# Kernel optimization log

Hardware: AMD Instinct MI355X
Metric: run time of the kernel (lower is better)

Reference implementation:

```python
import jax, jax.numpy as jnp
import numpy as np

N = 50000
E = 800000
C = 128          # in = hidden = out channels
R = 16           # num_relations
NB = 4           # num_bases
EPS = 1e-5


def setup_inputs() -> dict:
    key = jax.random.key(0)
    ks = jax.random.split(key, 20)
    node_features = jax.random.normal(ks[0], (N, C), dtype=jnp.float32)
    src = jax.random.randint(ks[1], (E,), 0, N, dtype=jnp.int32)
    rel = jax.random.randint(ks[2], (E,), 0, R, dtype=jnp.int32)
    dst = jax.random.randint(ks[3], (E,), 0, N, dtype=jnp.int32)
    edge_triples = jnp.stack([src, rel, dst], axis=1)  # [E,3]
    s = 0.05
    inp = {
        "node_features": node_features,
        "edge_triples": edge_triples,
        "num_nodes": N,
        "input_w": jax.random.normal(ks[4], (C, C), jnp.float32) * s,
        "input_b": jnp.zeros((C,), jnp.float32),
    }
    for i in range(2):
        k = jax.random.split(ks[5 + i], 4)
        inp[f"basis{i}"] = jax.random.normal(k[0], (NB, C, C), jnp.float32) * s
        inp[f"att{i}"] = jax.random.normal(k[1], (R, NB), jnp.float32) * s
        inp[f"root_w{i}"] = jax.random.normal(k[2], (C, C), jnp.float32) * s
        inp[f"root_b{i}"] = jnp.zeros((C,), jnp.float32)
        inp[f"ln_g{i}"] = jnp.ones((C,), jnp.float32)
        inp[f"ln_b{i}"] = jnp.zeros((C,), jnp.float32)
    return inp


def _layer_norm(x, g, b):
    mu = jnp.mean(x, axis=-1, keepdims=True)
    var = jnp.mean(jnp.square(x - mu), axis=-1, keepdims=True)
    return (x - mu) * jax.lax.rsqrt(var + EPS) * g + b


def _rel_conv(x, edge_triples, num_nodes, basis, att, root_w, root_b):
    # x: [N,C]; basis: [NB,C,O]; att: [R,NB]
    src = edge_triples[:, 0]
    rel = edge_triples[:, 1]
    dst = edge_triples[:, 2]
    # weights = einsum('rb,bio->rio'); messages_e = x[src] @ weights[rel]
    # = sum_b att[rel,b] * (x @ basis[b])[src]  (same math, no [E,C,O] tensor)
    xb = jnp.einsum('ni,bio->bno', x, basis)      # [NB,N,O]
    coef = att[rel]                                # [E,NB]
    out_dim = basis.shape[-1]
    msg = jnp.zeros((src.shape[0], out_dim), x.dtype)
    for b in range(basis.shape[0]):                # small fixed loop over bases
        msg = msg + coef[:, b, None] * xb[b][src]
    deg = jax.ops.segment_sum(jnp.ones_like(dst, dtype=x.dtype), dst,
                              num_segments=num_nodes)
    deg_inv = jnp.where(deg > 0, 1.0 / deg, 0.0)
    msg = msg * deg_inv[dst][:, None]
    out = jax.ops.segment_sum(msg, dst, num_segments=num_nodes)
    return out + x @ root_w + root_b


def reference(node_features, edge_triples, num_nodes, input_w, input_b,
              basis0, att0, root_w0, root_b0, ln_g0, ln_b0,
              basis1, att1, root_w1, root_b1, ln_g1, ln_b1):
    x = node_features @ input_w + input_b
    x = _rel_conv(x, edge_triples, num_nodes, basis0, att0, root_w0, root_b0)
    x = _layer_norm(x, ln_g0, ln_b0)
    x = jax.nn.relu(x)  # dropout is identity in eval mode
    x = _rel_conv(x, edge_triples, num_nodes, basis1, att1, root_w1, root_b1)
    x = _layer_norm(x, ln_g1, ln_b1)
    return x
```

## Files before the change

### kernel.cpp

```cpp
#include <hip/hip_runtime.h>
#include <hip/hip_bf16.h>
#include <hip/hip_fp8.h>

#define NN 50000
#define EE 800000
#define NBLK 196

typedef __bf16 bf16x8 __attribute__((ext_vector_type(8)));
typedef float f32x4 __attribute__((ext_vector_type(4)));

__device__ inline float bf2f(unsigned int u) {
    union { unsigned int i; float f; } x; x.i = (u & 0xFFFFu) << 16; return x.f;
}
__device__ inline float bf2fh(unsigned int u) {
    union { unsigned int i; float f; } x; x.i = u & 0xFFFF0000u; return x.f;
}
__device__ inline void bf8_to_f(bf16x8 v, float* f) {
    const unsigned int* u = (const unsigned int*)&v;
    f[0] = bf2f(u[0]); f[1] = bf2fh(u[0]);
    f[2] = bf2f(u[1]); f[3] = bf2fh(u[1]);
    f[4] = bf2f(u[2]); f[5] = bf2fh(u[2]);
    f[6] = bf2f(u[3]); f[7] = bf2fh(u[3]);
}

__device__ inline void fp8x8_to_f(uint2 w, float* f) {
#if __has_builtin(__builtin_amdgcn_cvt_f32_fp8)
    f[0] = __builtin_amdgcn_cvt_f32_fp8(w.x, 0);
    f[1] = __builtin_amdgcn_cvt_f32_fp8(w.x, 1);
    f[2] = __builtin_amdgcn_cvt_f32_fp8(w.x, 2);
    f[3] = __builtin_amdgcn_cvt_f32_fp8(w.x, 3);
    f[4] = __builtin_amdgcn_cvt_f32_fp8(w.y, 0);
    f[5] = __builtin_amdgcn_cvt_f32_fp8(w.y, 1);
    f[6] = __builtin_amdgcn_cvt_f32_fp8(w.y, 2);
    f[7] = __builtin_amdgcn_cvt_f32_fp8(w.y, 3);
#else
    const unsigned char* b = (const unsigned char*)&w;
    #pragma unroll
    for (int j = 0; j < 8; ++j) { __hip_fp8_e4m3 v; v.__x = b[j]; f[j] = float(v); }
#endif
}
__device__ inline uint2 f8_pack(const float* f) {
#if __has_builtin(__builtin_amdgcn_cvt_pk_fp8_f32)
    unsigned int lo = __builtin_amdgcn_cvt_pk_fp8_f32(f[0], f[1], 0u, false);
    lo = __builtin_amdgcn_cvt_pk_fp8_f32(f[2], f[3], lo, true);
    unsigned int hi = __builtin_amdgcn_cvt_pk_fp8_f32(f[4], f[5], 0u, false);
    hi = __builtin_amdgcn_cvt_pk_fp8_f32(f[6], f[7], hi, true);
    return make_uint2(lo, hi);
#else
    unsigned char b[8];
    #pragma unroll
    for (int j = 0; j < 8; ++j) { __hip_fp8_e4m3 v(f[j]); b[j] = v.__x; }
    return *(uint2*)b;
#endif
}

__global__ void k_cvt8(const __bf16* __restrict__ in, unsigned char* __restrict__ out, int n8) {
    int i = blockIdx.x * 256 + threadIdx.x;
    if (i >= n8) return;
    bf16x8 v = ((const bf16x8*)in)[i];
    float f[8];
    bf8_to_f(v, f);
    ((uint2*)out)[i] = f8_pack(f);
}

__global__ void k_zero(int* __restrict__ deg, int* __restrict__ curs) {
    int i = blockIdx.x * 256 + threadIdx.x;
    if (i < NN) { deg[i] = 0; curs[i] = 0; }
}

__global__ void k_deg(const int* __restrict__ et, int* __restrict__ deg) {
    int e = blockIdx.x * 256 + threadIdx.x;
    if (e < EE) atomicAdd(&deg[et[e * 3 + 2]], 1);
}

__global__ void k_scan1(const int* __restrict__ deg, int* __restrict__ incl, int* __restrict__ bsum) {
    __shared__ int s[1024];
    int i = blockIdx.x * 1024 + threadIdx.x;
    int v = (i < NN) ? deg[i] : 0;
    s[threadIdx.x] = v;
    __syncthreads();
    for (int off = 1; off < 1024; off <<= 1) {
        int t = (threadIdx.x >= off) ? s[threadIdx.x - off] : 0;
        __syncthreads();
        s[threadIdx.x] += t;
        __syncthreads();
    }
    if (i < NN) incl[i] = s[threadIdx.x];
    if (threadIdx.x == 1023) bsum[blockIdx.x] = s[1023];
}

__global__ void k_scan2(const int* __restrict__ bsum, int* __restrict__ boff) {
    if (threadIdx.x == 0 && blockIdx.x == 0) {
        int acc = 0;
        for (int i = 0; i < 49; ++i) { boff[i] = acc; acc += bsum[i]; }
    }
}

__global__ void k_scan3(const int* __restrict__ incl, const int* __restrict__ deg,
                        const int* __restrict__ boff, int* __restrict__ row_start) {
    int i = blockIdx.x * 1024 + threadIdx.x;
    if (i < NN) row_start[i] = incl[i] - deg[i] + boff[blockIdx.x];
}

__global__ void k_fill(const int* __restrict__ et, const int* __restrict__ row_start,
                       int* __restrict__ cursor, int* __restrict__ perm) {
    int e = blockIdx.x * 256 + threadIdx.x;
    if (e >= EE) return;
    int src = et[e * 3 + 0];
    int rel = et[e * 3 + 1];
    int dst = et[e * 3 + 2];
    int pos = row_start[dst] + atomicAdd(&cursor[dst], 1);
    perm[pos] = src | (rel << 16);
}

__global__ void k_prep(const float* __restrict__ iw,
                       const float* __restrict__ basis0, const float* __restrict__ rootw0,
                       const float* __restrict__ basis1, const float* __restrict__ rootw1,
                       __bf16* __restrict__ WtInF, __bf16* __restrict__ WtF0, __bf16* __restrict__ WtF1) {
    int t = blockIdx.x * 256 + threadIdx.x;
    if (t < 2048) {
        int lane = t & 63, grp = t >> 6;
        int kk = grp & 3, nblk = grp >> 2;
        int col = nblk * 16 + (lane & 15);
        int k0 = kk * 32 + (lane >> 4) * 8;
        bf16x8 v;
        #pragma unroll
        for (int j = 0; j < 8; ++j) v[j] = (__bf16)iw[(size_t)(k0 + j) * 128 + col];
        *(bf16x8*)(WtInF + (size_t)t * 8) = v;
        return;
    }
    t -= 2048;
    const float* basis = basis0; const float* rootw = rootw0; __bf16* W = WtF0;
    if (t >= 10240) { t -= 10240; basis = basis1; rootw = rootw1; W = WtF1; }
    if (t >= 10240) return;
    int lane = t & 63, grp = t >> 6;
    int kk = grp % 20, nblk = grp / 20;
    int col = nblk * 16 + (lane & 15);
    int k0 = kk * 32 + (lane >> 4) * 8;
    bf16x8 v;
    #pragma unroll
    for (int j = 0; j < 8; ++j) {
        int k = k0 + j;
        float f = (k < 512) ? basis[(size_t)(k >> 7) * 16384 + (size_t)(k & 127) * 128 + col]
                            : rootw[(size_t)(k - 512) * 128 + col];
        v[j] = (__bf16)f;
    }
    *(bf16x8*)(W + (size_t)t * 8) = v;
}

__global__ void k_gemm_in(const float* __restrict__ A, const __bf16* __restrict__ WtInF,
                          const float* __restrict__ bias, __bf16* __restrict__ out, int M) {
    const int tid = threadIdx.x, wave = tid >> 6, lane = tid & 63;
    const int wr = wave >> 1, wc = wave & 1;
    const int l15 = lane & 15, lhi = lane >> 4;
    f32x4 acc[2][4] = {};
    #define LDAI(dst, KK) do { \
        _Pragma("unroll") \
        for (int m = 0; m < 2; ++m) { \
            int rw = blockIdx.x * 64 + wr * 32 + m * 16 + l15; \
            rw = rw < M ? rw : M - 1; \
            const float* ap = A + (size_t)rw * 128 + (KK) * 32 + lhi * 8; \
            float4 v0 = *(const float4*)ap, v1 = *(const float4*)(ap + 4); \
            bf16x8 f; \
            f[0]=(__bf16)v0.x; f[1]=(__bf16)v0.y; f[2]=(__bf16)v0.z; f[3]=(__bf16)v0.w; \
            f[4]=(__bf16)v1.x; f[5]=(__bf16)v1.y; f[6]=(__bf16)v1.z; f[7]=(__bf16)v1.w; \
            dst[m] = f; \
        } } while (0)
    #define LDBI(dst, KK) do { \
        _Pragma("unroll") \
        for (int n = 0; n < 4; ++n) \
            dst[n] = *(const bf16x8*)(WtInF + (((size_t)(wc * 4 + n) * 4 + (KK)) * 64 + lane) * 8); \
        } while (0)
    #define MMI(AA, BB) do { \
        _Pragma("unroll") for (int m = 0; m < 2; ++m) \
        _Pragma("unroll") for (int n = 0; n < 4; ++n) \
            acc[m][n] = __builtin_amdgcn_mfma_f32_16x16x32_bf16(AA[m], BB[n], acc[m][n], 0, 0, 0); \
        } while (0)
    bf16x8 aP[2], bP[4], aQ[2], bQ[4];
    LDAI(aP, 0); LDBI(bP, 0);
    #pragma unroll
    for (int tstep = 0; tstep < 2; ++tstep) {
        LDAI(aQ, 2 * tstep + 1); LDBI(bQ, 2 * tstep + 1);
        MMI(aP, bP);
        if (tstep < 1) { LDAI(aP, 2 * tstep + 2); LDBI(bP, 2 * tstep + 2); }
        MMI(aQ, bQ);
    }
    #pragma unroll
    for (int m = 0; m < 2; ++m)
        #pragma unroll
        for (int j = 0; j < 4; ++j) {
            int row = blockIdx.x * 64 + wr * 32 + m * 16 + lhi * 4 + j;
            if (row >= M) continue;
            #pragma unroll
            for (int n = 0; n < 4; ++n) {
                int col = wc * 64 + n * 16 + l15;
                out[(size_t)row * 128 + col] = (__bf16)(acc[m][n][j] + bias[col]);
            }
        }
}

__global__ void k_agg7(const unsigned char* __restrict__ x8, const int* __restrict__ perm,
                       const int* __restrict__ rowst, const int* __restrict__ deg,
                       const float* __restrict__ att, __bf16* __restrict__ aggF,
                       int nodeOff, int nodeCnt) {
    __shared__ float4 satt[16];
    if (threadIdx.x < 16) satt[threadIdx.x] = ((const float4*)att)[threadIdx.x];
    __syncthreads();
    int local = blockIdx.x * 4 + (threadIdx.x >> 6);
    if (local >= nodeCnt) return;
    int lane = threadIdx.x & 63;
    int e4 = lane >> 4, c8 = lane & 15;
    int node = nodeOff + local;
    int start = rowst[node], cnt = deg[node];
    float acc[4][8] = {};
    int nIt = (cnt + 3) >> 2;
    for (int it = 0; it < nIt; it += 2) {
        int eA = it * 4 + e4, eB = eA + 4;
        bool vA = eA < cnt, vB = eB < cnt;
        int pA = vA ? perm[start + eA] : 0;
        int pB = vB ? perm[start + eB] : 0;
        uint2 uA = *(const uint2*)(x8 + (size_t)(pA & 0xFFFF) * 128 + c8 * 8);
        uint2 uB = *(const uint2*)(x8 + (size_t)(pB & 0xFFFF) * 128 + c8 * 8);
        float4 cA = vA ? satt[pA >> 16] : make_float4(0.f, 0.f, 0.f, 0.f);
        float4 cB = vB ? satt[pB >> 16] : make_float4(0.f, 0.f, 0.f, 0.f);
        float fA[8], fB[8];
        fp8x8_to_f(uA, fA);
        fp8x8_to_f(uB, fB);
        #pragma unroll
        for (int j = 0; j < 8; ++j) {
            acc[0][j] += cA.x * fA[j]; acc[1][j] += cA.y * fA[j];
            acc[2][j] += cA.z * fA[j]; acc[3][j] += cA.w * fA[j];
        }
        #pragma unroll
        for (int j = 0; j < 8; ++j) {
            acc[0][j] += cB.x * fB[j]; acc[1][j] += cB.y * fB[j];
            acc[2][j] += cB.z * fB[j]; acc[3][j] += cB.w * fB[j];
        }
    }
    float dinv = (cnt > 0) ? 1.f / (float)cnt : 0.f;
    #pragma unroll
    for (int b = 0; b < 4; ++b)
        #pragma unroll
        for (int j = 0; j < 8; ++j) {
            float v = acc[b][j];
            v += __shfl_xor(v, 16);
            v += __shfl_xor(v, 32);
            acc[b][j] = v * dinv;
        }
    bf16x8 o;
    #pragma unroll
    for (int j = 0; j < 8; ++j) {
        float v = (e4 == 0) ? acc[0][j] : (e4 == 1) ? acc[1][j] : (e4 == 2) ? acc[2][j] : acc[3][j];
        o[j] = (__bf16)v;
    }
    size_t idx8 = (((size_t)(local >> 4) * 16 + e4 * 4 + (c8 >> 2)) * 64 + (c8 & 3) * 16 + (local & 15)) * 8;
    *(bf16x8*)(aggF + idx8) = o;
}

template<int OUTF>
__global__ void k_gemm_layer(const __bf16* __restrict__ aggF, const __bf16* __restrict__ x,
                             const __bf16* __restrict__ WtF, const float* __restrict__ rb,
                             const float* __restrict__ g, const float* __restrict__ bb,
                             __bf16* __restrict__ outB, float* __restrict__ outF,
                             int rowOff, int nodeCnt) {
    __shared__ float red[2][2][64];
    __shared__ float murs[2][64];
    const int tid = threadIdx.x, wave = tid >> 6, lane = tid & 63;
    const int wr = wave >> 1, wc = wave & 1;
    const int l15 = lane & 15, lhi = lane >> 4;
    const int rowgrpBase = blockIdx.x * 4 + wr * 2;
    f32x4 acc[2][4] = {};
    #define LDA(dst, KK) do { \
        _Pragma("unroll") \
        for (int m = 0; m < 2; ++m) { \
            if ((KK) < 16) { \
                dst[m] = *(const bf16x8*)(aggF + (((size_t)(rowgrpBase + m) * 16 + (KK)) * 64 + lane) * 8); \
            } else { \
                int rw = blockIdx.x * 64 + wr * 32 + m * 16 + l15; \
                rw = rw < nodeCnt ? rw : nodeCnt - 1; \
                dst[m] = *(const bf16x8*)(x + (size_t)(rowOff + rw) * 128 + ((KK) - 16) * 32 + lhi * 8); \
            } \
        } } while (0)
    #define LDB(dst, KK) do { \
        _Pragma("unroll") \
        for (int n = 0; n < 4; ++n) \
            dst[n] = *(const bf16x8*)(WtF + (((size_t)(wc * 4 + n) * 20 + (KK)) * 64 + lane) * 8); \
        } while (0)
    #define MM(AA, BB) do { \
        _Pragma("unroll") for (int m = 0; m < 2; ++m) \
        _Pragma("unroll") for (int n = 0; n < 4; ++n) \
            acc[m][n] = __builtin_amdgcn_mfma_f32_16x16x32_bf16(AA[m], BB[n], acc[m][n], 0, 0, 0); \
        } while (0)
    bf16x8 aP[2], bP[4], aQ[2], bQ[4];
    LDA(aP, 0); LDB(bP, 0);
    #pragma unroll
    for (int t = 0; t < 10; ++t) {
        LDA(aQ, 2 * t + 1); LDB(bQ, 2 * t + 1);
        MM(aP, bP);
        if (t < 9) { LDA(aP, 2 * t + 2); LDB(bP, 2 * t + 2); }
        MM(aQ, bQ);
    }
    float colb[4];
    #pragma unroll
    for (int n = 0; n < 4; ++n) colb[n] = rb[wc * 64 + n * 16 + l15];
    #pragma unroll
    for (int m = 0; m < 2; ++m)
        #pragma unroll
        for (int j = 0; j < 4; ++j) {
            float s = 0.f, q = 0.f;
            #pragma unroll
            for (int n = 0; n < 4; ++n) {
                float v = acc[m][n][j] + colb[n];
                acc[m][n][j] = v;
                s += v; q += v * v;
            }
            #pragma unroll
            for (int o = 1; o < 16; o <<= 1) { s += __shfl_xor(s, o); q += __shfl_xor(q, o); }
            if (l15 == 0) {
                int r = wr * 32 + m * 16 + lhi * 4 + j;
                red[0][wc][r] = s; red[1][wc][r] = q;
            }
        }
    __syncthreads();
    if (tid < 64) {
        float s = red[0][0][tid] + red[0][1][tid];
        float q = red[1][0][tid] + red[1][1][tid];
        float mu = s * (1.f / 128.f);
        float var = q * (1.f / 128.f) - mu * mu;
        murs[0][tid] = mu;
        murs[1][tid] = rsqrtf(var + 1e-5f);
    }
    __syncthreads();
    float gg[4], gb[4];
    #pragma unroll
    for (int n = 0; n < 4; ++n) {
        int col = wc * 64 + n * 16 + l15;
        gg[n] = g[col]; gb[n] = bb[col];
    }
    #pragma unroll
    for (int m = 0; m < 2; ++m)
        #pragma unroll
        for (int j = 0; j < 4; ++j) {
            int rblk = wr * 32 + m * 16 + lhi * 4 + j;
            int lr = blockIdx.x * 64 + rblk;
            if (lr >= nodeCnt) continue;
            float mu = murs[0][rblk], rs = murs[1][rblk];
            size_t rowbase = (size_t)(rowOff + lr) * 128;
            #pragma unroll
            for (int n = 0; n < 4; ++n) {
                int col = wc * 64 + n * 16 + l15;
                float v = (acc[m][n][j] - mu) * rs * gg[n] + gb[n];
                if (OUTF == 0) { v = fmaxf(v, 0.f); outB[rowbase + col] = (__bf16)v; }
                else           { outF[rowbase + col] = v; }
            }
        }
}

extern "C" void kernel_launch(void* const* d_in, const int* in_sizes, int n_in,
                              void* d_out, int out_size, void* d_ws, size_t ws_size,
                              hipStream_t stream) {
    const float* nf      = (const float*)d_in[0];
    const int*   et      = (const int*)d_in[1];
    const float* input_w = (const float*)d_in[3];
    const float* input_b = (const float*)d_in[4];
    const float* basis0  = (const float*)d_in[5];
    const float* att0    = (const float*)d_in[6];
    const float* rootw0  = (const float*)d_in[7];
    const float* rootb0  = (const float*)d_in[8];
    const float* lng0    = (const float*)d_in[9];
    const float* lnb0    = (const float*)d_in[10];
    const float* basis1  = (const float*)d_in[11];
    const float* att1    = (const float*)d_in[12];
    const float* rootw1  = (const float*)d_in[13];
    const float* rootb1  = (const float*)d_in[14];
    const float* lng1    = (const float*)d_in[15];
    const float* lnb1    = (const float*)d_in[16];
    (void)in_sizes; (void)n_in; (void)out_size;

    char* ws = (char*)d_ws;
    size_t off = 0;
    auto carve = [&](size_t bytes) { char* p = ws + off; off = (off + bytes + 255) & ~(size_t)255; return p; };
    __bf16* x0    = (__bf16*)carve((size_t)NN * 128 * 2);
    __bf16* x1    = (__bf16*)carve((size_t)NN * 128 * 2);
    unsigned char* x08 = (unsigned char*)carve((size_t)NN * 128);
    unsigned char* x18 = (unsigned char*)carve((size_t)NN * 128);
    __bf16* WtInF = (__bf16*)carve((size_t)128 * 128 * 2);
    __bf16* WtF0  = (__bf16*)carve((size_t)128 * 640 * 2);
    __bf16* WtF1  = (__bf16*)carve((size_t)128 * 640 * 2);
    int*    deg   = (int*)carve((size_t)NN * 4);
    int*    incl  = (int*)carve((size_t)NN * 4);
    int*    rowst = (int*)carve((size_t)NN * 4);
    int*    curs  = (int*)carve((size_t)NN * 4);
    int*    bsum  = (int*)carve(64 * 4);
    int*    boff  = (int*)carve(64 * 4);
    int*    perm  = (int*)carve((size_t)EE * 4 + 64);
    size_t remain = (ws_size > off + 4096) ? (ws_size - off - 4096) : 0;
    long long maxNodes = (long long)(remain / 1024);
    int chunkN = (maxNodes >= NN) ? NN : (int)maxNodes;
    if (chunkN < 512) chunkN = 512;
    chunkN = (chunkN + 63) & ~63;
    __bf16* aggF = (__bf16*)carve((size_t)chunkN * 512 * 2);
    int nch = (NN + chunkN - 1) / chunkN;

    k_zero<<<NBLK, 256, 0, stream>>>(deg, curs);
    k_deg<<<(EE + 255) / 256, 256, 0, stream>>>(et, deg);
    k_scan1<<<49, 1024, 0, stream>>>(deg, incl, bsum);
    k_scan2<<<1, 64, 0, stream>>>(bsum, boff);
    k_scan3<<<49, 1024, 0, stream>>>(incl, deg, boff, rowst);
    k_fill<<<(EE + 255) / 256, 256, 0, stream>>>(et, rowst, curs, perm);

    k_prep<<<88, 256, 0, stream>>>(input_w, basis0, rootw0, basis1, rootw1, WtInF, WtF0, WtF1);
    k_gemm_in<<<(NN + 63) / 64, 256, 0, stream>>>(nf, WtInF, input_b, x0, NN);
    k_cvt8<<<(NN * 16 + 255) / 256, 256, 0, stream>>>(x0, x08, NN * 16);

    for (int c = 0; c < nch; ++c) {
        int o0 = c * chunkN;
        int cnt = (o0 + chunkN <= NN) ? chunkN : (NN - o0);
        k_agg7<<<(cnt + 3) / 4, 256, 0, stream>>>(x08, perm, rowst, deg, att0, aggF, o0, cnt);
        k_gemm_layer<0><<<(cnt + 63) / 64, 256, 0, stream>>>(aggF, x0, WtF0, rootb0, lng0, lnb0,
                                                             x1, nullptr, o0, cnt);
    }
    k_cvt8<<<(NN * 16 + 255) / 256, 256, 0, stream>>>(x1, x18, NN * 16);

    for (int c = 0; c < nch; ++c) {
        int o0 = c * chunkN;
        int cnt = (o0 + chunkN <= NN) ? chunkN : (NN - o0);
        k_agg7<<<(cnt + 3) / 4, 256, 0, stream>>>(x18, perm, rowst, deg, att1, aggF, o0, cnt);
        k_gemm_layer<1><<<(cnt + 63) / 64, 256, 0, stream>>>(aggF, x1, WtF1, rootb1, lng1, lnb1,
                                                             nullptr, (float*)d_out, o0, cnt);
    }
}
```

Baseline: 268.4 us.

## Fuse edge aggregation and basis GEMM with LayerNorm into one kernel

Merges the per-node fp8 gather/aggregation kernel and the MFMA GEMM+LayerNorm kernel into a single kernel per layer. Each 256-thread block aggregates 32 nodes into a shared-memory tile in MFMA fragment layout, then runs the GEMM and LayerNorm directly from LDS. This removes the global round-trip of the aggregated buffer and the chunked launch loop. In exchange, the GEMM tile per block shrinks from 64 to 32 rows, so weight fragments are reloaded twice as often, and about 33 KB of LDS per block limits occupancy.

```diff
diff --git a/kernel.cpp b/kernel.cpp
--- a/kernel.cpp
+++ b/kernel.cpp
@@ -199,130 +199,133 @@
         }
 }
 
-__global__ void k_agg7(const unsigned char* __restrict__ x8, const int* __restrict__ perm,
-                       const int* __restrict__ rowst, const int* __restrict__ deg,
-                       const float* __restrict__ att, __bf16* __restrict__ aggF,
-                       int nodeOff, int nodeCnt) {
+template<int OUTF>
+__global__ void __launch_bounds__(256, 4)
+k_fused(const unsigned char* __restrict__ x8, const __bf16* __restrict__ x,
+        const __bf16* __restrict__ WtF,
+        const int* __restrict__ perm, const int* __restrict__ rowst,
+        const int* __restrict__ deg, const float* __restrict__ att,
+        const float* __restrict__ rb, const float* __restrict__ g,
+        const float* __restrict__ bb,
+        __bf16* __restrict__ outB, float* __restrict__ outF)
+{
+    __shared__ __attribute__((aligned(16))) __bf16 aggL[32 * 512];
     __shared__ float4 satt[16];
-    if (threadIdx.x < 16) satt[threadIdx.x] = ((const float4*)att)[threadIdx.x];
+    __shared__ float red[2][2][32];
+    __shared__ float murs[2][32];
+    const int tid = threadIdx.x, wave = tid >> 6, lane = tid & 63;
+    if (tid < 16) satt[tid] = ((const float4*)att)[tid];
     __syncthreads();
-    int local = blockIdx.x * 4 + (threadIdx.x >> 6);
-    if (local >= nodeCnt) return;
-    int lane = threadIdx.x & 63;
-    int e4 = lane >> 4, c8 = lane & 15;
-    int node = nodeOff + local;
-    int start = rowst[node], cnt = deg[node];
-    float acc[4][8] = {};
-    int nIt = (cnt + 3) >> 2;
-    for (int it = 0; it < nIt; it += 2) {
-        int eA = it * 4 + e4, eB = eA + 4;
-        bool vA = eA < cnt, vB = eB < cnt;
-        int pA = vA ? perm[start + eA] : 0;
-        int pB = vB ? perm[start + eB] : 0;
-        uint2 uA = *(const uint2*)(x8 + (size_t)(pA & 0xFFFF) * 128 + c8 * 8);
-        uint2 uB = *(const uint2*)(x8 + (size_t)(pB & 0xFFFF) * 128 + c8 * 8);
-        float4 cA = vA ? satt[pA >> 16] : make_float4(0.f, 0.f, 0.f, 0.f);
-        float4 cB = vB ? satt[pB >> 16] : make_float4(0.f, 0.f, 0.f, 0.f);
-        float fA[8], fB[8];
-        fp8x8_to_f(uA, fA);
-        fp8x8_to_f(uB, fB);
-        #pragma unroll
-        for (int j = 0; j < 8; ++j) {
-            acc[0][j] += cA.x * fA[j]; acc[1][j] += cA.y * fA[j];
-            acc[2][j] += cA.z * fA[j]; acc[3][j] += cA.w * fA[j];
-        }
-        #pragma unroll
-        for (int j = 0; j < 8; ++j) {
-            acc[0][j] += cB.x * fB[j]; acc[1][j] += cB.y * fB[j];
-            acc[2][j] += cB.z * fB[j]; acc[3][j] += cB.w * fB[j];
-        }
-    }
-    float dinv = (cnt > 0) ? 1.f / (float)cnt : 0.f;
-    #pragma unroll
-    for (int b = 0; b < 4; ++b)
-        #pragma unroll
-        for (int j = 0; j < 8; ++j) {
-            float v = acc[b][j];
-            v += __shfl_xor(v, 16);
-            v += __shfl_xor(v, 32);
-            acc[b][j] = v * dinv;
-        }
-    bf16x8 o;
-    #pragma unroll
-    for (int j = 0; j < 8; ++j) {
-        float v = (e4 == 0) ? acc[0][j] : (e4 == 1) ? acc[1][j] : (e4 == 2) ? acc[2][j] : acc[3][j];
-        o[j] = (__bf16)v;
-    }
-    size_t idx8 = (((size_t)(local >> 4) * 16 + e4 * 4 + (c8 >> 2)) * 64 + (c8 & 3) * 16 + (local & 15)) * 8;
-    *(bf16x8*)(aggF + idx8) = o;
-}
-
-template<int OUTF>
-__global__ void k_gemm_layer(const __bf16* __restrict__ aggF, const __bf16* __restrict__ x,
-                             const __bf16* __restrict__ WtF, const float* __restrict__ rb,
-                             const float* __restrict__ g, const float* __restrict__ bb,
-                             __bf16* __restrict__ outB, float* __restrict__ outF,
-                             int rowOff, int nodeCnt) {
-    __shared__ float red[2][2][64];
-    __shared__ float murs[2][64];
-    const int tid = threadIdx.x, wave = tid >> 6, lane = tid & 63;
+    const int e4 = lane >> 4, c8 = lane & 15;
+    const int blockBase = blockIdx.x * 32;
+
+    for (int i = 0; i < 8; ++i) {
+        int local = wave * 8 + i;
+        int node = blockBase + local;
+        bf16x8 o;
+        #pragma unroll
+        for (int j = 0; j < 8; ++j) o[j] = (__bf16)0.f;
+        if (node < NN) {
+            int start = rowst[node], cnt = deg[node];
+            float acc[4][8] = {};
+            int nIt = (cnt + 3) >> 2;
+            for (int it = 0; it < nIt; it += 2) {
+                int eA = it * 4 + e4, eB = eA + 4;
+                bool vA = eA < cnt, vB = eB < cnt;
+                int pA = vA ? perm[start + eA] : 0;
+                int pB = vB ? perm[start + eB] : 0;
+                uint2 uA = *(const uint2*)(x8 + (size_t)(pA & 0xFFFF) * 128 + c8 * 8);
+                uint2 uB = *(const uint2*)(x8 + (size_t)(pB & 0xFFFF) * 128 + c8 * 8);
+                float4 cA = vA ? satt[pA >> 16] : make_float4(0.f, 0.f, 0.f, 0.f);
+                float4 cB = vB ? satt[pB >> 16] : make_float4(0.f, 0.f, 0.f, 0.f);
+                float fA[8], fB[8];
+                fp8x8_to_f(uA, fA);
+                fp8x8_to_f(uB, fB);
+                #pragma unroll
+                for (int j = 0; j < 8; ++j) {
+                    acc[0][j] += cA.x * fA[j]; acc[1][j] += cA.y * fA[j];
+                    acc[2][j] += cA.z * fA[j]; acc[3][j] += cA.w * fA[j];
+                }
+                #pragma unroll
+                for (int j = 0; j < 8; ++j) {
+                    acc[0][j] += cB.x * fB[j]; acc[1][j] += cB.y * fB[j];
+                    acc[2][j] += cB.z * fB[j]; acc[3][j] += cB.w * fB[j];
+                }
+            }
+            float dinv = (cnt > 0) ? 1.f / (float)cnt : 0.f;
+            #pragma unroll
+            for (int b = 0; b < 4; ++b)
+                #pragma unroll
+                for (int j = 0; j < 8; ++j) {
+                    float v = acc[b][j];
+                    v += __shfl_xor(v, 16);
+                    v += __shfl_xor(v, 32);
+                    acc[b][j] = v * dinv;
+                }
+            #pragma unroll
+            for (int j = 0; j < 8; ++j) {
+                float v = (e4 == 0) ? acc[0][j] : (e4 == 1) ? acc[1][j]
+                        : (e4 == 2) ? acc[2][j] : acc[3][j];
+                o[j] = (__bf16)v;
+            }
+        }
+        int idx8 = (((local >> 4) * 16 + e4 * 4 + (c8 >> 2)) * 64 + (c8 & 3) * 16 + (local & 15)) * 8;
+        *(bf16x8*)(aggL + idx8) = o;
+    }
+    __syncthreads();
+
     const int wr = wave >> 1, wc = wave & 1;
     const int l15 = lane & 15, lhi = lane >> 4;
-    const int rowgrpBase = blockIdx.x * 4 + wr * 2;
-    f32x4 acc[2][4] = {};
-    #define LDA(dst, KK) do { \
-        _Pragma("unroll") \
-        for (int m = 0; m < 2; ++m) { \
-            if ((KK) < 16) { \
-                dst[m] = *(const bf16x8*)(aggF + (((size_t)(rowgrpBase + m) * 16 + (KK)) * 64 + lane) * 8); \
-            } else { \
-                int rw = blockIdx.x * 64 + wr * 32 + m * 16 + l15; \
-                rw = rw < nodeCnt ? rw : nodeCnt - 1; \
-                dst[m] = *(const bf16x8*)(x + (size_t)(rowOff + rw) * 128 + ((KK) - 16) * 32 + lhi * 8); \
-            } \
+    f32x4 acc2[4] = {};
+    #define FLDA(dst, KK) do { \
+        if ((KK) < 16) { \
+            dst = *(const bf16x8*)(aggL + ((wr * 16 + (KK)) * 64 + lane) * 8); \
+        } else { \
+            int nd = blockBase + wr * 16 + l15; \
+            nd = nd < NN ? nd : NN - 1; \
+            dst = *(const bf16x8*)(x + (size_t)nd * 128 + ((KK) - 16) * 32 + lhi * 8); \
         } } while (0)
-    #define LDB(dst, KK) do { \
+    #define FLDB(dst, KK) do { \
         _Pragma("unroll") \
         for (int n = 0; n < 4; ++n) \
             dst[n] = *(const bf16x8*)(WtF + (((size_t)(wc * 4 + n) * 20 + (KK)) * 64 + lane) * 8); \
         } while (0)
-    #define MM(AA, BB) do { \
-        _Pragma("unroll") for (int m = 0; m < 2; ++m) \
+    #define FMM(AA, BB) do { \
         _Pragma("unroll") for (int n = 0; n < 4; ++n) \
-            acc[m][n] = __builtin_amdgcn_mfma_f32_16x16x32_bf16(AA[m], BB[n], acc[m][n], 0, 0, 0); \
+            acc2[n] = __builtin_amdgcn_mfma_f32_16x16x32_bf16(AA, BB[n], acc2[n], 0, 0, 0); \
         } while (0)
-    bf16x8 aP[2], bP[4], aQ[2], bQ[4];
-    LDA(aP, 0); LDB(bP, 0);
-    #pragma unroll
-    for (int t = 0; t < 10; ++t) {
-        LDA(aQ, 2 * t + 1); LDB(bQ, 2 * t + 1);
-        MM(aP, bP);
-        if (t < 9) { LDA(aP, 2 * t + 2); LDB(bP, 2 * t + 2); }
-        MM(aQ, bQ);
+    {
+        bf16x8 aP, bP[4], aQ, bQ[4];
+        FLDA(aP, 0); FLDB(bP, 0);
+        #pragma unroll
+        for (int t = 0; t < 10; ++t) {
+            FLDA(aQ, 2 * t + 1); FLDB(bQ, 2 * t + 1);
+            FMM(aP, bP);
+            if (t < 9) { FLDA(aP, 2 * t + 2); FLDB(bP, 2 * t + 2); }
+            FMM(aQ, bQ);
+        }
     }
     float colb[4];
     #pragma unroll
     for (int n = 0; n < 4; ++n) colb[n] = rb[wc * 64 + n * 16 + l15];
     #pragma unroll
-    for (int m = 0; m < 2; ++m)
-        #pragma unroll
-        for (int j = 0; j < 4; ++j) {
-            float s = 0.f, q = 0.f;
-            #pragma unroll
-            for (int n = 0; n < 4; ++n) {
-                float v = acc[m][n][j] + colb[n];
-                acc[m][n][j] = v;
-                s += v; q += v * v;
-            }
-            #pragma unroll
-            for (int o = 1; o < 16; o <<= 1) { s += __shfl_xor(s, o); q += __shfl_xor(q, o); }
-            if (l15 == 0) {
-                int r = wr * 32 + m * 16 + lhi * 4 + j;
-                red[0][wc][r] = s; red[1][wc][r] = q;
-            }
-        }
+    for (int j = 0; j < 4; ++j) {
+        float s = 0.f, q = 0.f;
+        #pragma unroll
+        for (int n = 0; n < 4; ++n) {
+            float v = acc2[n][j] + colb[n];
+            acc2[n][j] = v;
+            s += v; q += v * v;
+        }
+        #pragma unroll
+        for (int o = 1; o < 16; o <<= 1) { s += __shfl_xor(s, o); q += __shfl_xor(q, o); }
+        if (l15 == 0) {
+            int r = wr * 16 + lhi * 4 + j;
+            red[0][wc][r] = s; red[1][wc][r] = q;
+        }
+    }
     __syncthreads();
-    if (tid < 64) {
+    if (tid < 32) {
         float s = red[0][0][tid] + red[0][1][tid];
         float q = red[1][0][tid] + red[1][1][tid];
         float mu = s * (1.f / 128.f);
@@ -338,22 +341,20 @@
         gg[n] = g[col]; gb[n] = bb[col];
     }
     #pragma unroll
-    for (int m = 0; m < 2; ++m)
-        #pragma unroll
-        for (int j = 0; j < 4; ++j) {
-            int rblk = wr * 32 + m * 16 + lhi * 4 + j;
-            int lr = blockIdx.x * 64 + rblk;
-            if (lr >= nodeCnt) continue;
-            float mu = murs[0][rblk], rs = murs[1][rblk];
-            size_t rowbase = (size_t)(rowOff + lr) * 128;
-            #pragma unroll
-            for (int n = 0; n < 4; ++n) {
-                int col = wc * 64 + n * 16 + l15;
-                float v = (acc[m][n][j] - mu) * rs * gg[n] + gb[n];
-                if (OUTF == 0) { v = fmaxf(v, 0.f); outB[rowbase + col] = (__bf16)v; }
-                else           { outF[rowbase + col] = v; }
-            }
-        }
+    for (int j = 0; j < 4; ++j) {
+        int rblk = wr * 16 + lhi * 4 + j;
+        int node = blockBase + rblk;
+        if (node >= NN) continue;
+        float mu = murs[0][rblk], rs = murs[1][rblk];
+        size_t rowbase = (size_t)node * 128;
+        #pragma unroll
+        for (int n = 0; n < 4; ++n) {
+            int col = wc * 64 + n * 16 + l15;
+            float v = (acc2[n][j] - mu) * rs * gg[n] + gb[n];
+            if (OUTF == 0) { v = fmaxf(v, 0.f); outB[rowbase + col] = (__bf16)v; }
+            else           { outF[rowbase + col] = v; }
+        }
+    }
 }
 
 extern "C" void kernel_launch(void* const* d_in, const int* in_sizes, int n_in,
@@ -375,7 +376,7 @@
     const float* rootb1  = (const float*)d_in[14];
     const float* lng1    = (const float*)d_in[15];
     const float* lnb1    = (const float*)d_in[16];
-    (void)in_sizes; (void)n_in; (void)out_size;
+    (void)in_sizes; (void)n_in; (void)out_size; (void)ws_size;
 
     char* ws = (char*)d_ws;
     size_t off = 0;
@@ -394,13 +395,6 @@
     int*    bsum  = (int*)carve(64 * 4);
     int*    boff  = (int*)carve(64 * 4);
     int*    perm  = (int*)carve((size_t)EE * 4 + 64);
-    size_t remain = (ws_size > off + 4096) ? (ws_size - off - 4096) : 0;
-    long long maxNodes = (long long)(remain / 1024);
-    int chunkN = (maxNodes >= NN) ? NN : (int)maxNodes;
-    if (chunkN < 512) chunkN = 512;
-    chunkN = (chunkN + 63) & ~63;
-    __bf16* aggF = (__bf16*)carve((size_t)chunkN * 512 * 2);
-    int nch = (NN + chunkN - 1) / chunkN;
 
     k_zero<<<NBLK, 256, 0, stream>>>(deg, curs);
     k_deg<<<(EE + 255) / 256, 256, 0, stream>>>(et, deg);
@@ -413,20 +407,10 @@
     k_gemm_in<<<(NN + 63) / 64, 256, 0, stream>>>(nf, WtInF, input_b, x0, NN);
     k_cvt8<<<(NN * 16 + 255) / 256, 256, 0, stream>>>(x0, x08, NN * 16);
 
-    for (int c = 0; c < nch; ++c) {
-        int o0 = c * chunkN;
-        int cnt = (o0 + chunkN <= NN) ? chunkN : (NN - o0);
-        k_agg7<<<(cnt + 3) / 4, 256, 0, stream>>>(x08, perm, rowst, deg, att0, aggF, o0, cnt);
-        k_gemm_layer<0><<<(cnt + 63) / 64, 256, 0, stream>>>(aggF, x0, WtF0, rootb0, lng0, lnb0,
-                                                             x1, nullptr, o0, cnt);
-    }
+    const int fblocks = (NN + 31) / 32;
+    k_fused<0><<<fblocks, 256, 0, stream>>>(x08, x0, WtF0, perm, rowst, deg, att0,
+                                            rootb0, lng0, lnb0, x1, nullptr);
     k_cvt8<<<(NN * 16 + 255) / 256, 256, 0, stream>>>(x1, x18, NN * 16);
-
-    for (int c = 0; c < nch; ++c) {
-        int o0 = c * chunkN;
-        int cnt = (o0 + chunkN <= NN) ? chunkN : (NN - o0);
-        k_agg7<<<(cnt + 3) / 4, 256, 0, stream>>>(x18, perm, rowst, deg, att1, aggF, o0, cnt);
-        k_gemm_layer<1><<<(cnt + 63) / 64, 256, 0, stream>>>(aggF, x1, WtF1, rootb1, lng1, lnb1,
-                                                             nullptr, (float*)d_out, o0, cnt);
-    }
-}
+    k_fused<1><<<fblocks, 256, 0, stream>>>(x18, x1, WtF1, perm, rowst, deg, att1,
+                                            rootb1, lng1, lnb1, nullptr, (float*)d_out);
+}
```

Measured after the change: 301.0 us. 12.2% more time.
